# Kernel optimization log

Measured on AMD Instinct MI355X. Metric: run time of the kernel, lower is better.

The kernel has to match this reference:

```python
import jax, jax.numpy as jnp
import numpy as np
import math

EPS = 1e-20
TEMP = 0.07


def _affinity(x1, x2, n):
    # x1, x2: (B, C, T-1, N+1); use only the first n (non-dustbin) nodes
    A = jnp.einsum('bctn,bctm->btnm', x1[..., :n], x2[..., :n])  # (B,T-1,n,n)
    # entropy of row-normalized affinities (intended math of Categorical(probs=A[b,t,k]).entropy())
    p = A / A.sum(-1, keepdims=True)
    ent = -(p * jnp.log(jnp.maximum(p, EPS))).sum(-1)            # (B,T-1,n)
    dustbin_w = 1.0 / math.log(n)
    A = jnp.concatenate([A, (ent * dustbin_w)[..., None]], axis=-1)  # (B,T-1,n,n+1)
    dust_row = -A.sum(-2)[:, :, None, :]                              # (B,T-1,1,n+1)
    A = jnp.concatenate([A, dust_row], axis=2)                        # (B,T-1,n+1,n+1)
    A = A.at[:, :, -1, -1].set(0.0)
    return A


def _l2norm(x, axis):
    return x / jnp.maximum(jnp.linalg.norm(x, axis=axis, keepdims=True), 1e-12)


def _forward(feats_raw, dust_raw, W_self, b_self, W_dust, b_dust):
    B, N, Cenc, T = feats_raw.shape
    # selfsim head: Linear over channel dim, then L2-normalize features
    f = jnp.einsum('bnct,cd->bndt', feats_raw, W_self) + b_self[None, None, :, None]
    f = _l2norm(f, axis=2)                      # (B,N,128,T)
    q = jnp.transpose(f, (0, 2, 3, 1))          # (B,128,T,N)
    d = jnp.einsum('bct,cd->bdt', dust_raw, W_dust) + b_dust[None, :, None]
    d = _l2norm(d, axis=1)                      # (B,128,T)
    q = jnp.concatenate([q, d[..., None]], axis=-1)  # (B,128,T,N+1)

    Af = _affinity(q[:, :, :-1], q[:, :, 1:], N)
    qf = jnp.flip(q, axis=2)
    Ab = _affinity(qf[:, :, :-1], qf[:, :, 1:], N)

    A12 = jax.nn.softmax(Af / TEMP, axis=-1)    # (B,T-1,M,M)
    A21 = jax.nn.softmax(Ab / TEMP, axis=-1)

    M = N + 1
    tgt = jnp.tile(jnp.arange(M), B)            # (B*M,)
    rows = jnp.arange(B * M)
    left = A12[:, 0]
    right = A21[:, T - 2]
    losses = []
    for i in range(1, T - 1):                   # fixed small loop over time steps
        left = left @ A12[:, i]
        right = A21[:, T - 2 - i] @ right
        AA = left @ right                       # (B,M,M) palindrome walk
        logits = jnp.log(AA + EPS).reshape(-1, M)
        ls = jax.nn.log_softmax(logits, axis=-1)
        losses.append(-ls[rows, tgt].mean())
    loss = sum(losses) / len(losses)
    return q, loss


def setup_inputs() -> dict:
    key = jax.random.key(0)
    ks = jax.random.split(key, 4)
    B, N, C, T, D = 4, 784, 512, 8, 128
    return {
        'feats_raw': jax.random.normal(ks[0], (B, N, C, T), dtype=jnp.float32),
        'dust_raw': jax.random.normal(ks[1], (B, C, T), dtype=jnp.float32),
        'W_self': jax.random.normal(ks[2], (C, D), dtype=jnp.float32) * 0.05,
        'b_self': jnp.zeros((D,), dtype=jnp.float32),
        'W_dust': jax.random.normal(ks[3], (C, D), dtype=jnp.float32) * 0.05,
        'b_dust': jnp.zeros((D,), dtype=jnp.float32),
    }


def reference(feats_raw, dust_raw, W_self, b_self, W_dust, b_dust):
    return _forward(feats_raw, dust_raw, W_self, b_self, W_dust, b_dust)
```

## Files before the change

kernel.cpp:

```cpp
#include <hip/hip_runtime.h>
#include <hip/hip_bf16.h>
#include <math.h>

constexpr int Bc = 4;
constexpr int Nc = 784;
constexpr int Cc = 512;
constexpr int Tc = 8;
constexpr int Dc = 128;
constexpr int Mc = 785;
constexpr int TM1 = 7;
constexpr int Pp = 832;
constexpr int Qrows = 896;
constexpr float TEMP = 0.07f;

typedef __attribute__((ext_vector_type(4))) float f32x4;
typedef __attribute__((ext_vector_type(8))) unsigned short u16x8;
typedef __attribute__((ext_vector_type(8))) __bf16 bf16x8;

__device__ __forceinline__ unsigned short f2bf(float v) {
    __hip_bfloat16 h = __float2bfloat16(v);
    return __builtin_bit_cast(unsigned short, h);
}
__device__ __forceinline__ float bf2f(unsigned short u) {
    return __builtin_bit_cast(float, (unsigned int)u << 16);
}

__device__ __forceinline__ void gload16(const void* g, void* l) {
    __builtin_amdgcn_global_load_lds(
        (const __attribute__((address_space(1))) unsigned int*)g,
        (__attribute__((address_space(3))) unsigned int*)l, 16, 0, 0);
}

template<int LD>
__device__ __forceinline__ void mfma_tile_loop(const unsigned short* __restrict__ A,
                                               const unsigned short* __restrict__ BT,
                                               unsigned short* __restrict__ As,
                                               unsigned short* __restrict__ Bs,
                                               int i0, int j0, int tid,
                                               f32x4 (&acc)[4][4])
{
    const int lane = tid & 63, w = tid >> 6;
    const int wr = w >> 1, wc = w & 1;
    const int g = lane >> 4, lr = lane & 15;

    for (int k0 = 0; k0 < LD; k0 += 64) {
        __syncthreads();
        #pragma unroll
        for (int q = 0; q < 4; ++q) {
            int L16 = q * 256 + tid;
            int r = L16 >> 3;
            int csw = ((L16 & 7) << 4) ^ ((r & 7) << 4);
            const char* ga = (const char*)(A  + (size_t)(i0 + r) * LD + k0) + csw;
            const char* gb = (const char*)(BT + (size_t)(j0 + r) * LD + k0) + csw;
            gload16(ga, As + (size_t)L16 * 8);
            gload16(gb, Bs + (size_t)L16 * 8);
        }
        __syncthreads();
        #pragma unroll
        for (int ks = 0; ks < 2; ++ks) {
            bf16x8 af[4], bf[4];
            #pragma unroll
            for (int m = 0; m < 4; ++m) {
                int r = wr * 64 + m * 16 + lr;
                int cb = (ks * 64 + g * 16) ^ ((r & 7) << 4);
                af[m] = __builtin_bit_cast(bf16x8, *(const u16x8*)((const char*)As + r * 128 + cb));
            }
            #pragma unroll
            for (int n = 0; n < 4; ++n) {
                int r = wc * 64 + n * 16 + lr;
                int cb = (ks * 64 + g * 16) ^ ((r & 7) << 4);
                bf[n] = __builtin_bit_cast(bf16x8, *(const u16x8*)((const char*)Bs + r * 128 + cb));
            }
            #pragma unroll
            for (int m = 0; m < 4; ++m)
                #pragma unroll
                for (int n = 0; n < 4; ++n)
                    acc[m][n] = __builtin_amdgcn_mfma_f32_16x16x32_bf16(af[m], bf[n], acc[m][n], 0, 0, 0);
        }
    }
}

__device__ __forceinline__ float blockReduceSum(float v, float* sbuf) {
    #pragma unroll
    for (int off = 32; off; off >>= 1) v += __shfl_down(v, off, 64);
    __syncthreads();
    if ((threadIdx.x & 63) == 0) sbuf[threadIdx.x >> 6] = v;
    __syncthreads();
    return sbuf[0] + sbuf[1] + sbuf[2] + sbuf[3];
}
__device__ __forceinline__ float blockReduceMax(float v, float* sbuf) {
    #pragma unroll
    for (int off = 32; off; off >>= 1) v = fmaxf(v, __shfl_down(v, off, 64));
    __syncthreads();
    if ((threadIdx.x & 63) == 0) sbuf[threadIdx.x >> 6] = v;
    __syncthreads();
    return fmaxf(fmaxf(sbuf[0], sbuf[1]), fmaxf(sbuf[2], sbuf[3]));
}

__global__ __launch_bounds__(256) void k_pack(const float* __restrict__ feats,
                                              unsigned int* __restrict__ Abf32)
{
    __shared__ float lds[Cc * 9];
    int bid = blockIdx.x;
    int b = bid / Nc, n = bid % Nc;
    const float* src = feats + (size_t)(b * Nc + n) * Cc * Tc;
    int tid = threadIdx.x;
    for (int i = tid; i < Cc * Tc; i += 256) lds[(i >> 3) * 9 + (i & 7)] = src[i];
    __syncthreads();
    #pragma unroll
    for (int t = 0; t < Tc; ++t) {
        size_t row = (size_t)(b * Tc + t) * Nc + n;
        float v0 = lds[(2 * tid) * 9 + t];
        float v1 = lds[(2 * tid + 1) * 9 + t];
        unsigned int pk = (unsigned int)f2bf(v0) | ((unsigned int)f2bf(v1) << 16);
        Abf32[row * (Cc / 2) + tid] = pk;
    }
}

__global__ __launch_bounds__(256) void k_packw(const float* __restrict__ Wself,
                                               const float* __restrict__ Wdust,
                                               unsigned short* __restrict__ WTb)
{
    __shared__ float tile[64][65];
    int which = blockIdx.z;
    const float* W = which ? Wdust : Wself;
    unsigned short* O = WTb + (size_t)which * Dc * Cc;
    int d0 = blockIdx.x * 64, c0 = blockIdx.y * 64;
    int tx = threadIdx.x & 63, ty = threadIdx.x >> 6;
    #pragma unroll
    for (int y = 0; y < 64; y += 4) tile[y + ty][tx] = W[(size_t)(c0 + y + ty) * Dc + d0 + tx];
    __syncthreads();
    #pragma unroll
    for (int y = 0; y < 64; y += 4) O[(size_t)(d0 + y + ty) * Cc + c0 + tx] = f2bf(tile[tx][y + ty]);
}

__global__ __launch_bounds__(256, 3) void k_gemm_proj(const unsigned short* __restrict__ A,
                                                      const unsigned short* __restrict__ BT,
                                                      const float* __restrict__ bias,
                                                      float* __restrict__ Cf)
{
    __shared__ __align__(16) unsigned short As[128 * 64];
    __shared__ __align__(16) unsigned short Bs[128 * 64];
    const int i0 = blockIdx.y * 128;
    const int tid = threadIdx.x, lane = tid & 63, w = tid >> 6;
    const int wr = w >> 1, wc = w & 1;
    const int g = lane >> 4, lr = lane & 15;

    f32x4 acc[4][4] = {};
    mfma_tile_loop<Cc>(A, BT, As, Bs, i0, 0, tid, acc);

    #pragma unroll
    for (int n = 0; n < 4; ++n) {
        int col = wc * 64 + n * 16 + lr;
        float bv = bias[col];
        #pragma unroll
        for (int m = 0; m < 4; ++m)
            #pragma unroll
            for (int j = 0; j < 4; ++j) {
                int row = i0 + wr * 64 + m * 16 + g * 4 + j;
                Cf[(size_t)row * Dc + col] = acc[m][n][j] + bv;
            }
    }
}

__global__ __launch_bounds__(128) void k_dustproj(const float* __restrict__ dust,
                                                  const float* __restrict__ Wdust,
                                                  const float* __restrict__ bdust,
                                                  unsigned short* __restrict__ qTb,
                                                  float* __restrict__ qout)
{
    __shared__ float sdust[Cc];
    __shared__ float red[2];
    int bt = blockIdx.x;
    int b = bt >> 3, t = bt & 7;
    int tid = threadIdx.x;
    for (int i = tid; i < Cc; i += 128) sdust[i] = dust[((size_t)b * Cc + i) * Tc + t];
    __syncthreads();
    float acc = 0.f;
    for (int c = 0; c < Cc; ++c) acc += sdust[c] * Wdust[(size_t)c * Dc + tid];
    acc += bdust[tid];
    float s = acc * acc;
    #pragma unroll
    for (int off = 32; off; off >>= 1) s += __shfl_down(s, off, 64);
    if ((tid & 63) == 0) red[tid >> 6] = s;
    __syncthreads();
    float inv = 1.f / fmaxf(sqrtf(red[0] + red[1]), 1e-12f);
    float qv = acc * inv;
    qTb[((size_t)bt * Qrows + Nc) * Dc + tid] = f2bf(qv);
    qout[(((size_t)b * Dc + tid) * Tc + t) * Mc + Nc] = qv;
}

__global__ __launch_bounds__(256) void k_norm(const float* __restrict__ fbuf,
                                              unsigned short* __restrict__ qTb,
                                              float* __restrict__ qout)
{
    __shared__ float lds[64][129];
    __shared__ float nrm[64][4];
    __shared__ float inv[64];
    int bt = blockIdx.y;
    int b = bt >> 3, t = bt & 7;
    int n0 = blockIdx.x * 64;
    int tid = threadIdx.x;
    #pragma unroll
    for (int q = 0; q < 8; ++q) {
        int i = q * 256 + tid;
        int nl = i >> 5, d4 = i & 31;
        f32x4 v = {};
        if (n0 + nl < Nc) v = *(const f32x4*)(fbuf + ((size_t)bt * Nc + n0 + nl) * Dc + d4 * 4);
        *(f32x4*)(&lds[nl][d4 * 4]) = v;
    }
    __syncthreads();
    {
        int r = tid & 63, p = tid >> 6;
        float s = 0.f;
        #pragma unroll
        for (int j = 0; j < 32; ++j) { float v = lds[r][p * 32 + j]; s += v * v; }
        nrm[r][p] = s;
    }
    __syncthreads();
    if (tid < 64) inv[tid] = 1.f / fmaxf(sqrtf(nrm[tid][0] + nrm[tid][1] + nrm[tid][2] + nrm[tid][3]), 1e-12f);
    __syncthreads();
    unsigned int* qT32 = (unsigned int*)(qTb + (size_t)bt * Qrows * Dc);
    #pragma unroll
    for (int q = 0; q < 16; ++q) {
        int i = q * 256 + tid;
        int nl = i >> 6, dp = i & 63;
        if (n0 + nl < Nc) {
            float iv = inv[nl];
            unsigned int pk = (unsigned int)f2bf(lds[nl][2 * dp] * iv)
                            | ((unsigned int)f2bf(lds[nl][2 * dp + 1] * iv) << 16);
            qT32[((size_t)(n0 + nl) * Dc >> 1) + dp] = pk;
        }
    }
    int nl = tid & 63;
    if (n0 + nl < Nc) {
        float iv = inv[nl];
        #pragma unroll
        for (int dd = 0; dd < Dc; dd += 4) {
            int d = dd + (tid >> 6);
            qout[(((size_t)b * Dc + d) * Tc + t) * Mc + n0 + nl] = lds[nl][d] * iv;
        }
    }
}

__global__ __launch_bounds__(256) void k_affinity(const unsigned short* __restrict__ qTb,
                                                  unsigned short* __restrict__ P12h,
                                                  unsigned short* __restrict__ P21h,
                                                  float* __restrict__ cs12,
                                                  float* __restrict__ cs21,
                                                  float wconst)
{
    constexpr float INVT = 1.0f / TEMP;
    const size_t MMp = (size_t)Pp * Pp;
    __shared__ unsigned short otile[16][840];
    __shared__ float sred[16][4][2];
    __shared__ float rowsum[16], invZ[16], entP[16];

    int f = blockIdx.x;
    int xcd = f & 7, slot = f >> 3;
    int grp = xcd + 8 * (slot / 49);
    int strip = slot % 49;
    int side = grp >= 28 ? 1 : 0;
    int bt = grp - side * 28;
    int b = bt / TM1, t = bt % TM1;
    const unsigned short *Aq, *Bq;
    unsigned short* OUT;
    if (side == 0) {
        Aq = qTb + (size_t)(b * Tc + t)     * Qrows * Dc;
        Bq = qTb + (size_t)(b * Tc + t + 1) * Qrows * Dc;
        OUT = P12h + (size_t)bt * MMp;
    } else {
        Aq = qTb + (size_t)(b * Tc + 7 - t) * Qrows * Dc;
        Bq = qTb + (size_t)(b * Tc + 6 - t) * Qrows * Dc;
        OUT = P21h + (size_t)bt * MMp;
    }
    float* csFlip = (side == 0 ? cs21 : cs12) + (size_t)(b * TM1 + (6 - t)) * Pp;

    const int r0 = strip * 16;
    const int tid = threadIdx.x, lane = tid & 63, w = tid >> 6;
    const int g = lane >> 4, lr = lane & 15;

    f32x4 acc[13] = {};
    #pragma unroll
    for (int ks = 0; ks < 4; ++ks) {
        bf16x8 af = __builtin_bit_cast(bf16x8,
            *(const u16x8*)(Aq + (size_t)(r0 + lr) * Dc + ks * 32 + g * 8));
        bf16x8 bfr[7];
        #pragma unroll
        for (int tt = 0; tt < 7; ++tt)
            if (w * 13 + tt < 49)
                bfr[tt] = __builtin_bit_cast(bf16x8,
                    *(const u16x8*)(Bq + (size_t)((w * 13 + tt) * 16 + lr) * Dc + ks * 32 + g * 8));
        #pragma unroll
        for (int tt = 0; tt < 7; ++tt)
            if (w * 13 + tt < 49)
                acc[tt] = __builtin_amdgcn_mfma_f32_16x16x32_bf16(af, bfr[tt], acc[tt], 0, 0, 0);
        #pragma unroll
        for (int tt = 7; tt < 13; ++tt)
            if (w * 13 + tt < 49)
                bfr[tt - 7] = __builtin_bit_cast(bf16x8,
                    *(const u16x8*)(Bq + (size_t)((w * 13 + tt) * 16 + lr) * Dc + ks * 32 + g * 8));
        #pragma unroll
        for (int tt = 7; tt < 13; ++tt)
            if (w * 13 + tt < 49)
                acc[tt] = __builtin_amdgcn_mfma_f32_16x16x32_bf16(af, bfr[tt - 7], acc[tt], 0, 0, 0);
    }

    float rs[4] = {0.f, 0.f, 0.f, 0.f};
    #pragma unroll
    for (int tt = 0; tt < 13; ++tt) {
        if (w * 13 + tt < 49) {
            #pragma unroll
            for (int j = 0; j < 4; ++j) rs[j] += acc[tt][j];
        }
    }
    #pragma unroll
    for (int off = 1; off <= 8; off <<= 1) {
        #pragma unroll
        for (int j = 0; j < 4; ++j) rs[j] += __shfl_xor(rs[j], off, 64);
    }
    if (lr == 0) {
        #pragma unroll
        for (int j = 0; j < 4; ++j) sred[g * 4 + j][w][0] = rs[j];
    }
    __syncthreads();
    if (tid < 16) {
        float r = sred[tid][0][0] + sred[tid][1][0] + sred[tid][2][0] + sred[tid][3][0];
        rowsum[tid] = r;
        csFlip[r0 + tid] = r;
    }
    __syncthreads();

    float invr[4];
    #pragma unroll
    for (int j = 0; j < 4; ++j) invr[j] = 1.0f / rowsum[g * 4 + j];
    float en[4] = {0.f, 0.f, 0.f, 0.f}, es[4] = {0.f, 0.f, 0.f, 0.f};
    #pragma unroll
    for (int tt = 0; tt < 13; ++tt) {
        if (w * 13 + tt < 49) {
            #pragma unroll
            for (int j = 0; j < 4; ++j) {
                float a = acc[tt][j];
                float e = __expf(a * INVT);
                es[j] += e;
                float p = a * invr[j];
                en[j] -= p * __logf(fmaxf(p, 1e-20f));
                acc[tt][j] = e;
            }
        }
    }
    #pragma unroll
    for (int off = 1; off <= 8; off <<= 1) {
        #pragma unroll
        for (int j = 0; j < 4; ++j) {
            es[j] += __shfl_xor(es[j], off, 64);
            en[j] += __shfl_xor(en[j], off, 64);
        }
    }
    if (lr == 0) {
        #pragma unroll
        for (int j = 0; j < 4; ++j) { sred[g * 4 + j][w][0] = es[j]; sred[g * 4 + j][w][1] = en[j]; }
    }
    __syncthreads();
    if (tid < 16) {
        float esum = sred[tid][0][0] + sred[tid][1][0] + sred[tid][2][0] + sred[tid][3][0];
        float ent  = sred[tid][0][1] + sred[tid][1][1] + sred[tid][2][1] + sred[tid][3][1];
        float ez  = __expf(ent * wconst * INVT);
        float Z   = esum + ez;
        float iz  = 1.0f / Z;
        invZ[tid] = iz;
        entP[tid] = ez * iz;
    }
    __syncthreads();

    float izl[4];
    #pragma unroll
    for (int j = 0; j < 4; ++j) izl[j] = invZ[g * 4 + j];
    #pragma unroll
    for (int tt = 0; tt < 13; ++tt) {
        int gt = w * 13 + tt;
        if (gt < 49) {
            int col = gt * 16 + lr;
            #pragma unroll
            for (int j = 0; j < 4; ++j)
                otile[g * 4 + j][col] = f2bf(acc[tt][j] * izl[j]);
        }
    }
    if (tid < 16) otile[tid][784] = f2bf(entP[tid]);
    for (int i = tid; i < 16 * 47; i += 256) otile[i / 47][785 + i % 47] = 0;
    __syncthreads();

    for (int v = tid; v < 16 * 104; v += 256) {
        int row = v / 104, cv = v % 104;
        *(u16x8*)(OUT + (size_t)(r0 + row) * Pp + cv * 8) = *(const u16x8*)(&otile[row][cv * 8]);
    }
}

__global__ __launch_bounds__(256) void k_dustrow(const float* __restrict__ cs12,
                                                 const float* __restrict__ cs21,
                                                 unsigned short* __restrict__ P12h,
                                                 unsigned short* __restrict__ P21h)
{
    constexpr float INVT = 1.0f / TEMP;
    const size_t MMp = (size_t)Pp * Pp;
    int bt = blockIdx.x, side = blockIdx.y;
    const float* cs = (side ? cs21 : cs12) + (size_t)bt * Pp;
    unsigned short* OUT = (side ? P21h : P12h) + (size_t)bt * MMp;
    __shared__ float sbuf[4];
    int tid = threadIdx.x;
    float v[4];
    #pragma unroll
    for (int k = 0; k < 4; ++k) {
        int j = tid + k * 256;
        float val = -INFINITY;
        if (j < Nc)       val = -cs[j] * INVT;
        else if (j == Nc) val = 0.f;
        v[k] = val;
    }
    float mx = fmaxf(fmaxf(v[0], v[1]), fmaxf(v[2], v[3]));
    mx = blockReduceMax(mx, sbuf);
    float e[4]; float s = 0.f;
    #pragma unroll
    for (int k = 0; k < 4; ++k) {
        int j = tid + k * 256;
        e[k] = (j < Mc) ? __expf(v[k] - mx) : 0.f;
        s += e[k];
    }
    s = blockReduceSum(s, sbuf);
    float invs = 1.f / s;
    #pragma unroll
    for (int k = 0; k < 4; ++k) {
        int j = tid + k * 256;
        if (j < Mc)      OUT[(size_t)Nc * Pp + j] = f2bf(e[k] * invs);
        else if (j < Pp) OUT[(size_t)Nc * Pp + j] = 0;
    }
    u16x8 z = {};
    u16x8* dst = (u16x8*)(OUT + (size_t)785 * Pp);
    for (int i = tid; i < (Pp - 785) * Pp / 8; i += 256) dst[i] = z;
}

__global__ __launch_bounds__(256) void k_transpose_bf16(const unsigned short* __restrict__ P12h,
                                                        const unsigned short* __restrict__ P21h,
                                                        unsigned short* __restrict__ Db)
{
    const size_t MMp = (size_t)Pp * Pp;
    __shared__ unsigned short tile[64][65];
    int z = blockIdx.z;
    const unsigned short* S;
    if (z < 24) { int b = z / 6, tm = z % 6; S = P12h + ((size_t)b * 7 + tm + 1) * MMp; }
    else        { S = P21h + ((size_t)(z - 24) * 7 + 6) * MMp; }
    unsigned short* D = Db + (size_t)z * MMp;
    int x0 = blockIdx.x * 64, y0 = blockIdx.y * 64;
    int tx = threadIdx.x & 63, ty = threadIdx.x >> 6;
    #pragma unroll
    for (int y = 0; y < 64; y += 4) tile[y + ty][tx] = S[(size_t)(y0 + y + ty) * Pp + x0 + tx];
    __syncthreads();
    #pragma unroll
    for (int y = 0; y < 64; y += 4) D[(size_t)(x0 + y + ty) * Pp + y0 + tx] = tile[tx][y + ty];
}

struct GJobs {
    const unsigned short* A[2];
    const unsigned short* BT[2];
    unsigned short* Cb[2];
    float* cs[2];
    long long sA[2], sB[2], sC[2];
    const unsigned short* Lr;
    const unsigned short* Rr;
    const float* csL;
    float* loss;
    float scale;
};

__global__ __launch_bounds__(256, 4) void k_gemm_loss(GJobs J)
{
    const size_t MMp = (size_t)Pp * Pp;
    if (blockIdx.x >= 728) {
        int q = blockIdx.x - 728;
        int w = threadIdx.x >> 6, lane = threadIdx.x & 63;
        int r = q * 4 + w;
        int b = r / Mc, i = r % Mc;
        const u16x8* lrow = (const u16x8*)(J.Lr + (size_t)b * MMp + (size_t)i * Pp);
        const u16x8* rrow = (const u16x8*)(J.Rr + (size_t)b * MMp + (size_t)i * Pp);
        const f32x4* cs4  = (const f32x4*)(J.csL + (size_t)b * Pp);
        float sR = 0.f, sD = 0.f;
        for (int c = lane; c < Pp / 8; c += 64) {
            u16x8 lv = lrow[c];
            u16x8 rv = rrow[c];
            f32x4 c0 = cs4[2 * c], c1 = cs4[2 * c + 1];
            #pragma unroll
            for (int k = 0; k < 4; ++k) {
                float fl = bf2f(lv[k]);
                sR += fl * c0[k];
                sD += fl * bf2f(rv[k]);
            }
            #pragma unroll
            for (int k = 0; k < 4; ++k) {
                float fl = bf2f(lv[4 + k]);
                sR += fl * c1[k];
                sD += fl * bf2f(rv[4 + k]);
            }
        }
        #pragma unroll
        for (int off = 1; off <= 32; off <<= 1) {
            sR += __shfl_xor(sR, off, 64);
            sD += __shfl_xor(sD, off, 64);
        }
        if (lane == 0)
            atomicAdd(J.loss, (logf(sR + Mc * 1e-20f) - logf(sD + 1e-20f)) * J.scale);
        return;
    }

    __shared__ __align__(16) unsigned short As[64 * 64];
    __shared__ __align__(16) unsigned short Bs[128 * 64];

    int f = blockIdx.x;
    int zz = f & 7, slot = f >> 3;
    int job = zz >> 2, b = zz & 3;
    const unsigned short* A  = J.A[job]  + (size_t)b * J.sA[job];
    const unsigned short* BT = J.BT[job] + (size_t)b * J.sB[job];

    const int i0 = (slot / 7) * 64, j0 = (slot % 7) * 128;
    const int tid = threadIdx.x, lane = tid & 63, wv = tid >> 6;
    const int g = lane >> 4, lr = lane & 15;

    f32x4 acc[4][2] = {};

    for (int k0 = 0; k0 < Pp; k0 += 64) {
        __syncthreads();
        #pragma unroll
        for (int q = 0; q < 2; ++q) {
            int s = q * 256 + tid;
            int r = s >> 3;
            int csw = ((s & 7) << 4) ^ ((r & 7) << 4);
            gload16((const char*)(A + (size_t)(i0 + r) * Pp + k0) + csw, As + (size_t)s * 8);
        }
        #pragma unroll
        for (int q = 0; q < 4; ++q) {
            int s = q * 256 + tid;
            int r = s >> 3;
            int csw = ((s & 7) << 4) ^ ((r & 7) << 4);
            gload16((const char*)(BT + (size_t)(j0 + r) * Pp + k0) + csw, Bs + (size_t)s * 8);
        }
        __syncthreads();
        #pragma unroll
        for (int ks = 0; ks < 2; ++ks) {
            bf16x8 af[4], bf[2];
            #pragma unroll
            for (int m = 0; m < 4; ++m) {
                int r = m * 16 + lr;
                int cb = (ks * 64 + g * 16) ^ ((r & 7) << 4);
                af[m] = __builtin_bit_cast(bf16x8, *(const u16x8*)((const char*)As + r * 128 + cb));
            }
            #pragma unroll
            for (int n = 0; n < 2; ++n) {
                int r = wv * 32 + n * 16 + lr;
                int cb = (ks * 64 + g * 16) ^ ((r & 7) << 4);
                bf[n] = __builtin_bit_cast(bf16x8, *(const u16x8*)((const char*)Bs + r * 128 + cb));
            }
            #pragma unroll
            for (int m = 0; m < 4; ++m)
                #pragma unroll
                for (int n = 0; n < 2; ++n)
                    acc[m][n] = __builtin_amdgcn_mfma_f32_16x16x32_bf16(af[m], bf[n], acc[m][n], 0, 0, 0);
        }
    }

    unsigned short* Co = J.Cb[job] + (size_t)b * J.sC[job];
    float* csp = J.cs[job];
    float csacc[2] = {0.f, 0.f};
    #pragma unroll
    for (int m = 0; m < 4; ++m)
        #pragma unroll
        for (int n = 0; n < 2; ++n)
            #pragma unroll
            for (int j = 0; j < 4; ++j) {
                int row = i0 + m * 16 + g * 4 + j;
                int col = j0 + wv * 32 + n * 16 + lr;
                if (col < Pp) {
                    unsigned short h = f2bf(acc[m][n][j]);
                    Co[(size_t)row * Pp + col] = h;
                    csacc[n] += bf2f(h);
                }
            }
    if (csp) {
        csp += (size_t)b * Pp;
        #pragma unroll
        for (int n = 0; n < 2; ++n) {
            float p = csacc[n];
            p += __shfl_xor(p, 16, 64);
            p += __shfl_xor(p, 32, 64);
            int col = j0 + wv * 32 + n * 16 + lr;
            if (g == 0 && col < Pp) atomicAdd(&csp[col], p);
        }
    }
}

__global__ __launch_bounds__(64) void k_lossrow(const unsigned short* __restrict__ L,
                                                const unsigned short* __restrict__ R,
                                                const float* __restrict__ csR,
                                                float* __restrict__ loss, float scale)
{
    const size_t MMp = (size_t)Pp * Pp;
    int r = blockIdx.x;
    int b = r / Mc, i = r % Mc;
    const u16x8* lrow = (const u16x8*)(L + (size_t)b * MMp + (size_t)i * Pp);
    const u16x8* rrow = (const u16x8*)(R + (size_t)b * MMp + (size_t)i * Pp);
    const f32x4* cs4  = (const f32x4*)(csR + (size_t)b * Pp);
    int lane = threadIdx.x;
    float sR = 0.f, sD = 0.f;
    for (int c = lane; c < Pp / 8; c += 64) {
        u16x8 lv = lrow[c];
        u16x8 rv = rrow[c];
        f32x4 c0 = cs4[2 * c], c1 = cs4[2 * c + 1];
        #pragma unroll
        for (int k = 0; k < 4; ++k) {
            float fl = bf2f(lv[k]);
            sR += fl * c0[k];
            sD += fl * bf2f(rv[k]);
        }
        #pragma unroll
        for (int k = 0; k < 4; ++k) {
            float fl = bf2f(lv[4 + k]);
            sR += fl * c1[k];
            sD += fl * bf2f(rv[4 + k]);
        }
    }
    #pragma unroll
    for (int off = 1; off <= 32; off <<= 1) {
        sR += __shfl_xor(sR, off, 64);
        sD += __shfl_xor(sD, off, 64);
    }
    if (lane == 0)
        atomicAdd(loss, (logf(sR + Mc * 1e-20f) - logf(sD + 1e-20f)) * scale);
}

extern "C" void kernel_launch(void* const* d_in, const int* in_sizes, int n_in,
                              void* d_out, int out_size, void* d_ws, size_t ws_size,
                              hipStream_t stream)
{
    const float* feats = (const float*)d_in[0];
    const float* dust  = (const float*)d_in[1];
    const float* Wself = (const float*)d_in[2];
    const float* bself = (const float*)d_in[3];
    const float* Wdust = (const float*)d_in[4];
    const float* bdust = (const float*)d_in[5];

    float* out  = (float*)d_out;
    float* qout = out;
    float* loss = out + (size_t)Bc * Dc * Tc * Mc;

    const size_t MMp = (size_t)Pp * Pp;

    float* ws = (float*)d_ws;
    float* csR = ws;
    unsigned short* P12h = (unsigned short*)(ws + 4 * MMp);
    unsigned short* P21h = P12h + (size_t)28 * MMp;
    unsigned short* chainT = P21h + (size_t)28 * MMp;
    unsigned short* P12T  = chainT;
    unsigned short* P21T6 = P12T + (size_t)24 * MMp;
    unsigned short* l0    = P21T6 + (size_t)4 * MMp;
    unsigned short* l1    = l0 + (size_t)4 * MMp;
    unsigned short* R0    = l1 + (size_t)4 * MMp;
    unsigned short* R1    = R0 + (size_t)4 * MMp;
    unsigned short* qTb   = R1 + (size_t)4 * MMp;
    float* cs12 = (float*)(qTb + (size_t)32 * Qrows * Dc);
    float* cs21 = cs12 + (size_t)28 * Pp;

    unsigned short* Abf   = chainT;
    unsigned int*   Abf32 = (unsigned int*)Abf;
    unsigned short* WTb   = Abf + (size_t)Bc * Tc * Nc * Cc;
    float*          fbuf  = (float*)(WTb + 2 * (size_t)Dc * Cc);

    k_pack<<<Bc * Nc, 256, 0, stream>>>(feats, Abf32);
    k_packw<<<dim3(2, 8, 2), 256, 0, stream>>>(Wself, Wdust, WTb);
    hipMemsetAsync(csR, 0, (size_t)6 * Bc * Pp * sizeof(float), stream);
    hipMemsetAsync(loss, 0, sizeof(float), stream);
    k_gemm_proj<<<dim3(1, 196), 256, 0, stream>>>(Abf, WTb, bself, fbuf);
    k_dustproj<<<32, 128, 0, stream>>>(dust, Wdust, bdust, qTb, qout);
    k_norm<<<dim3(13, 32), 256, 0, stream>>>(fbuf, qTb, qout);
    float wconst = (float)(1.0 / log(784.0));
    k_affinity<<<2744, 256, 0, stream>>>(qTb, P12h, P21h, cs12, cs21, wconst);
    k_dustrow<<<dim3(28, 2), 256, 0, stream>>>(cs12, cs21, P12h, P21h);
    k_transpose_bf16<<<dim3(13, 13, 28), 256, 0, stream>>>(P12h, P21h, P12T);

    const float scale = 1.0f / (6.0f * Bc * Mc);

    {
        GJobs J = {};
        J.A[0] = P12h;  J.sA[0] = (long long)7 * MMp;
        J.BT[0] = P12T; J.sB[0] = (long long)6 * MMp;
        J.Cb[0] = l0;   J.sC[0] = (long long)MMp; J.cs[0] = nullptr;
        J.A[1] = P21T6;                   J.sA[1] = (long long)MMp;
        J.BT[1] = P21h + (size_t)5 * MMp; J.sB[1] = (long long)7 * MMp;
        J.Cb[1] = R0;   J.sC[1] = (long long)MMp; J.cs[1] = csR;
        k_gemm_loss<<<728, 256, 0, stream>>>(J);
    }

    unsigned short *lcur = l0, *lnxt = l1, *rcur = R0, *rnxt = R1;
    for (int i = 1; i <= 5; ++i) {
        GJobs J = {};
        J.A[0] = lcur; J.sA[0] = (long long)MMp;
        J.BT[0] = P12T + (size_t)i * MMp; J.sB[0] = (long long)6 * MMp;
        J.Cb[0] = lnxt; J.sC[0] = (long long)MMp; J.cs[0] = nullptr;
        J.A[1] = rcur; J.sA[1] = (long long)MMp;
        J.BT[1] = P21h + (size_t)(5 - i) * MMp; J.sB[1] = (long long)7 * MMp;
        J.Cb[1] = rnxt; J.sC[1] = (long long)MMp; J.cs[1] = csR + (size_t)i * Bc * Pp;
        J.Lr = lcur; J.Rr = rcur; J.csL = csR + (size_t)(i - 1) * Bc * Pp;
        J.loss = loss; J.scale = scale;
        k_gemm_loss<<<728 + 785, 256, 0, stream>>>(J);
        unsigned short* t;
        t = lcur; lcur = lnxt; lnxt = t;
        t = rcur; rcur = rnxt; rnxt = t;
    }
    k_lossrow<<<Bc * Mc, 64, 0, stream>>>(lcur, rcur, csR + (size_t)5 * Bc * Pp, loss, scale);
}
```

Baseline: 481.6 us.

## Overlap next K-tile global loads with MFMA in chained-walk GEMM; cap affinity occupancy

The bf16 GEMM main loop now reads a whole 64-wide K slice from LDS into registers, then issues the next tile's global-to-LDS loads before running the MFMAs. This lets memory traffic overlap with matrix math inside a single LDS buffer. The affinity kernel also gets a launch bound of two blocks per CU, which constrains its register allocation. In exchange the loop holds more fragment registers and keeps two barriers per iteration, and the occupancy hint may force spills.

```diff
diff --git a/kernel.cpp b/kernel.cpp
--- a/kernel.cpp
+++ b/kernel.cpp
@@ -243,12 +243,12 @@
     }
 }
 
-__global__ __launch_bounds__(256) void k_affinity(const unsigned short* __restrict__ qTb,
-                                                  unsigned short* __restrict__ P12h,
-                                                  unsigned short* __restrict__ P21h,
-                                                  float* __restrict__ cs12,
-                                                  float* __restrict__ cs21,
-                                                  float wconst)
+__global__ __launch_bounds__(256, 2) void k_affinity(const unsigned short* __restrict__ qTb,
+                                                     unsigned short* __restrict__ P12h,
+                                                     unsigned short* __restrict__ P21h,
+                                                     float* __restrict__ cs12,
+                                                     float* __restrict__ cs21,
+                                                     float wconst)
 {
     constexpr float INVT = 1.0f / TEMP;
     const size_t MMp = (size_t)Pp * Pp;
@@ -526,44 +526,65 @@
 
     f32x4 acc[4][2] = {};
 
-    for (int k0 = 0; k0 < Pp; k0 += 64) {
-        __syncthreads();
-        #pragma unroll
-        for (int q = 0; q < 2; ++q) {
-            int s = q * 256 + tid;
-            int r = s >> 3;
-            int csw = ((s & 7) << 4) ^ ((r & 7) << 4);
-            gload16((const char*)(A + (size_t)(i0 + r) * Pp + k0) + csw, As + (size_t)s * 8);
-        }
-        #pragma unroll
-        for (int q = 0; q < 4; ++q) {
-            int s = q * 256 + tid;
-            int r = s >> 3;
-            int csw = ((s & 7) << 4) ^ ((r & 7) << 4);
-            gload16((const char*)(BT + (size_t)(j0 + r) * Pp + k0) + csw, Bs + (size_t)s * 8);
-        }
-        __syncthreads();
+    #pragma unroll
+    for (int q = 0; q < 2; ++q) {
+        int s = q * 256 + tid;
+        int r = s >> 3;
+        int csw = ((s & 7) << 4) ^ ((r & 7) << 4);
+        gload16((const char*)(A + (size_t)(i0 + r) * Pp) + csw, As + (size_t)s * 8);
+    }
+    #pragma unroll
+    for (int q = 0; q < 4; ++q) {
+        int s = q * 256 + tid;
+        int r = s >> 3;
+        int csw = ((s & 7) << 4) ^ ((r & 7) << 4);
+        gload16((const char*)(BT + (size_t)(j0 + r) * Pp) + csw, Bs + (size_t)s * 8);
+    }
+    __syncthreads();
+
+    for (int t = 0; t < 13; ++t) {
+        bf16x8 af[2][4], bf[2][2];
         #pragma unroll
         for (int ks = 0; ks < 2; ++ks) {
-            bf16x8 af[4], bf[2];
             #pragma unroll
             for (int m = 0; m < 4; ++m) {
                 int r = m * 16 + lr;
                 int cb = (ks * 64 + g * 16) ^ ((r & 7) << 4);
-                af[m] = __builtin_bit_cast(bf16x8, *(const u16x8*)((const char*)As + r * 128 + cb));
+                af[ks][m] = __builtin_bit_cast(bf16x8, *(const u16x8*)((const char*)As + r * 128 + cb));
             }
             #pragma unroll
             for (int n = 0; n < 2; ++n) {
                 int r = wv * 32 + n * 16 + lr;
                 int cb = (ks * 64 + g * 16) ^ ((r & 7) << 4);
-                bf[n] = __builtin_bit_cast(bf16x8, *(const u16x8*)((const char*)Bs + r * 128 + cb));
-            }
+                bf[ks][n] = __builtin_bit_cast(bf16x8, *(const u16x8*)((const char*)Bs + r * 128 + cb));
+            }
+        }
+        __syncthreads();
+        if (t < 12) {
+            int k0 = (t + 1) * 64;
+            #pragma unroll
+            for (int q = 0; q < 2; ++q) {
+                int s = q * 256 + tid;
+                int r = s >> 3;
+                int csw = ((s & 7) << 4) ^ ((r & 7) << 4);
+                gload16((const char*)(A + (size_t)(i0 + r) * Pp + k0) + csw, As + (size_t)s * 8);
+            }
+            #pragma unroll
+            for (int q = 0; q < 4; ++q) {
+                int s = q * 256 + tid;
+                int r = s >> 3;
+                int csw = ((s & 7) << 4) ^ ((r & 7) << 4);
+                gload16((const char*)(BT + (size_t)(j0 + r) * Pp + k0) + csw, Bs + (size_t)s * 8);
+            }
+        }
+        #pragma unroll
+        for (int ks = 0; ks < 2; ++ks)
             #pragma unroll
             for (int m = 0; m < 4; ++m)
                 #pragma unroll
                 for (int n = 0; n < 2; ++n)
-                    acc[m][n] = __builtin_amdgcn_mfma_f32_16x16x32_bf16(af[m], bf[n], acc[m][n], 0, 0, 0);
-        }
+                    acc[m][n] = __builtin_amdgcn_mfma_f32_16x16x32_bf16(af[ks][m], bf[ks][n], acc[m][n], 0, 0, 0);
+        __syncthreads();
     }
 
     unsigned short* Co = J.Cb[job] + (size_t)b * J.sC[job];
```

After: 470.6 us. 1.02x faster.
